# Kernel tuning notes

Hardware: AMD Instinct MI355X
Metric: run time of the kernel (lower is better)

Reference implementation:

```python
import jax, jax.numpy as jnp
import numpy as np

MGC_SIZE = 80
COND_DIM = 256
LSTM_SIZE = 500
UP_SCALE = 64  # prod([4,4,4])
TEMPERATURE = 1.0
EPS_MIN = -7.0


def setup_inputs() -> dict:
    key = jax.random.key(0)
    ks = jax.random.split(key, 10)
    B, T_FRAMES = 16, 32
    T = T_FRAMES * UP_SCALE  # 2048 decode steps
    s = 0.02  # weight scale for numerical stability (logvar goes through exp)
    return {
        "mgc": jax.random.normal(ks[0], (B, T_FRAMES, MGC_SIZE), dtype=jnp.float32),
        "eps": jax.random.normal(ks[1], (B, T), dtype=jnp.float32),
        # UpsampleNet stand-in: linear projection mgc_size->256, then repeat x64 in time
        "W_up": jax.random.normal(ks[2], (MGC_SIZE, COND_DIM), dtype=jnp.float32) * s,
        "b_up": jnp.zeros((COND_DIM,), dtype=jnp.float32),
        # LSTM (PyTorch layout, gate order i,f,g,o)
        "W_ih": jax.random.normal(ks[3], (4 * LSTM_SIZE, COND_DIM + 1), dtype=jnp.float32) * s,
        "W_hh": jax.random.normal(ks[4], (4 * LSTM_SIZE, LSTM_SIZE), dtype=jnp.float32) * s,
        "b_ih": jax.random.normal(ks[5], (4 * LSTM_SIZE,), dtype=jnp.float32) * s,
        "b_hh": jax.random.normal(ks[6], (4 * LSTM_SIZE,), dtype=jnp.float32) * s,
        # output Linear(lstm_size, 2)
        "W_out": jax.random.normal(ks[7], (2, LSTM_SIZE), dtype=jnp.float32) * s,
        "b_out": jnp.zeros((2,), dtype=jnp.float32),
    }


def reference(mgc, eps, W_up, b_up, W_ih, W_hh, b_ih, b_hh, W_out, b_out):
    B = mgc.shape[0]
    # conditioning: (B, T_frames, 80) -> (B, T, 256)
    cond = jnp.repeat(mgc @ W_up + b_up, UP_SCALE, axis=1)
    bias = b_ih + b_hh

    def step(carry, xs):
        h, c, x_prev = carry              # (B,H), (B,H), (B,)
        cond_t, eps_t = xs                # (B,256), (B,)
        inp = jnp.concatenate([cond_t, x_prev[:, None]], axis=1)  # (B,257)
        gates = inp @ W_ih.T + h @ W_hh.T + bias                  # (B,4H)
        i, f, g, o = jnp.split(gates, 4, axis=1)
        i = jax.nn.sigmoid(i)
        f = jax.nn.sigmoid(f)
        g = jnp.tanh(g)
        o = jax.nn.sigmoid(o)
        c = f * c + i * g
        h = o * jnp.tanh(c)
        out = h @ W_out.T + b_out         # (B,2)
        mean = jnp.tanh(out[:, 0])
        logvar = jnp.maximum(out[:, 1], EPS_MIN)  # clamp(min=eps_min)
        zz = mean + (eps_t * TEMPERATURE) * jnp.exp(logvar)
        return (h, c, zz), (mean, logvar, zz)

    h0 = jnp.zeros((B, LSTM_SIZE), dtype=mgc.dtype)
    c0 = jnp.zeros((B, LSTM_SIZE), dtype=mgc.dtype)
    x0 = jnp.zeros((B,), dtype=mgc.dtype)
    xs = (cond.transpose(1, 0, 2), eps.T)  # time-major
    _, (mean, logvar, zz) = jax.lax.scan(step, (h0, c0, x0), xs)
    # back to (B, T)
    return mean.T, logvar.T, zz.T
```

## Files before the change

### kernel.cpp

```cpp
#include <hip/hip_runtime.h>
#include <stdint.h>

#define TSTEPS 2048
#define NB     16
#define HDIM   500
#define HPAD   512
#define NSLICE 16
#define NTHR   256
#define RECU32 320

typedef __attribute__((ext_vector_type(8))) short s16x8;
typedef __attribute__((ext_vector_type(4))) float f32x4;

__device__ __forceinline__ unsigned short f2bf(float f) {
    unsigned u = __float_as_uint(f);
    u += 0x7FFFu + ((u >> 16) & 1u);
    return (unsigned short)(u >> 16);
}
__device__ __forceinline__ float sigm(float x)   { return __fdividef(1.f, 1.f + __expf(-x)); }
__device__ __forceinline__ float tanhf_(float x) { return 1.f - __fdividef(2.f, __expf(2.f * x) + 1.f); }

__global__ void zero_ws_kernel(uint32_t* p, int n) {
    int i = blockIdx.x * blockDim.x + threadIdx.x;
    if (i < n) p[i] = 0u;
}

__global__ __launch_bounds__(NTHR, 1) void wavernn_persist(
    const float* __restrict__ mgc,  const float* __restrict__ eps,
    const float* __restrict__ Wup,  const float* __restrict__ bup,
    const float* __restrict__ Wih,  const float* __restrict__ Whh,
    const float* __restrict__ bih,  const float* __restrict__ bhh,
    const float* __restrict__ Wout, const float* __restrict__ bout,
    float* __restrict__ out, uint32_t* __restrict__ hbuf, uint32_t* __restrict__ seq)
{
    const int s    = blockIdx.x;
    const int tid  = threadIdx.x;
    const int lane = tid & 63;
    const int wave = tid >> 6;
    const int l16  = lane & 15;
    const int g    = lane >> 4;

    __shared__ __align__(16) uint32_t h_sw[HPAD * NB / 2];
    __shared__ __align__(16) float gates_l[NB * 132];
    __shared__ __align__(16) float gcond[128 * NB];
    __shared__ __align__(16) float condT[256 * NB];
    __shared__ __align__(16) float mgcl[NB * 80];
    __shared__ __align__(16) float eps_l[64 * NB];

    s16x8 bfr[2][16];
    float wihl[2];
    #pragma unroll
    for (int t2 = 0; t2 < 2; ++t2) {
        const int q    = t2 * 16 + l16;
        const int hidx = s * 32 + q;
        const bool valid = hidx < HDIM;
        const int grow = wave * HDIM + hidx;
        wihl[t2] = valid ? Wih[grow * 257 + 256] : 0.f;
        #pragma unroll
        for (int kk = 0; kk < 16; ++kk) {
            const int k0 = kk * 32 + g * 8;
            s16x8 r;
            #pragma unroll
            for (int j = 0; j < 8; ++j) {
                const int k = k0 + j;
                const float v = (valid && k < HDIM) ? Whh[grow * HDIM + k] : 0.f;
                r[j] = (short)f2bf(v);
            }
            bfr[t2][kk] = r;
        }
    }
    const int b_e = tid >> 4;
    const int qh  = tid & 15;
    const int q0  = 2 * qh, q1 = q0 + 1;
    const int k0g = s * 32 + q0, k1g = s * 32 + q1;
    const float w0q0 = (k0g < HDIM) ? Wout[k0g]        : 0.f;
    const float w0q1 = (k1g < HDIM) ? Wout[k1g]        : 0.f;
    const float w1q0 = (k0g < HDIM) ? Wout[HDIM + k0g] : 0.f;
    const float w1q1 = (k1g < HDIM) ? Wout[HDIM + k1g] : 0.f;
    const float bout0 = bout[0], bout1 = bout[1];
    float cst0 = 0.f, cst1 = 0.f;

    for (int t = 0; t < TSTEPS; ++t) {
        if (t > 0) {
            int guard = 0;
            while (__hip_atomic_load(&seq[(tid & 15) * 32], __ATOMIC_RELAXED,
                                     __HIP_MEMORY_SCOPE_AGENT) < (uint32_t)t) {
                if (++guard > (1 << 20)) break;
            }
        }
        __threadfence();

        {
            const int b = tid >> 4, p = tid & 15;
            const uint32_t gbase = (uint32_t)((((t & 1) ^ 1) * 16 + p) * RECU32 + b * 16);
            const uint4* srcp = (const uint4*)&hbuf[gbase];
            uint4 v0 = srcp[0], v1 = srcp[1], v2 = srcp[2], v3 = srcp[3];
            const int sw = (b & 7) << 4;
            char* hb = (char*)h_sw;
            *(uint4*)(hb + ((b * 1024 + p * 64 +  0) ^ sw)) = v0;
            *(uint4*)(hb + ((b * 1024 + p * 64 + 16) ^ sw)) = v1;
            *(uint4*)(hb + ((b * 1024 + p * 64 + 32) ^ sw)) = v2;
            *(uint4*)(hb + ((b * 1024 + p * 64 + 48) ^ sw)) = v3;
        }
        float zzv = 0.f, mean = 0.f, lv = 0.f;
        {
            const int b = tid & 15;
            float o0 = bout0, o1 = bout1;
            #pragma unroll
            for (int j = 0; j < 16; ++j) {
                const float2 pp = *(const float2*)&hbuf[(((t & 1) ^ 1) * 16 + j) * RECU32 + 256 + b * 2];
                o0 += pp.x; o1 += pp.y;
            }
            if (t > 0) {
                mean = tanhf_(o0);
                lv   = fmaxf(o1, -7.f);
                zzv  = mean + eps_l[((t - 1) & 63) * NB + b] * __expf(lv);
            }
        }
        if (s == 0 && t > 0 && tid < 16) {
            out[         tid * 2048 + (t - 1)] = mean;
            out[32768 +  tid * 2048 + (t - 1)] = lv;
            out[65536 +  tid * 2048 + (t - 1)] = zzv;
        }
        __syncthreads();

        if ((t & 63) == 0) {
            const int f = t >> 6;
            for (int i = tid; i < NB * 80; i += NTHR) {
                const int b = i / 80, m = i - b * 80;
                mgcl[i] = mgc[(b * 32 + f) * 80 + m];
            }
            for (int i = tid; i < 64 * NB; i += NTHR) {
                const int st = i >> 4, b = i & 15;
                eps_l[i] = eps[b * 2048 + f * 64 + st];
            }
            __syncthreads();
            {
                const int c = tid;
                float a[NB];
                #pragma unroll
                for (int b = 0; b < NB; ++b) a[b] = bup[c];
                for (int m = 0; m < 80; ++m) {
                    const float w = Wup[m * 256 + c];
                    #pragma unroll
                    for (int b = 0; b < NB; ++b) a[b] += mgcl[b * 80 + m] * w;
                }
                #pragma unroll
                for (int b = 0; b < NB; ++b) condT[c * NB + b] = a[b];
            }
            __syncthreads();
            {
                const int n = tid >> 1, kc = tid & 1;
                const int gate = n >> 5, q = n & 31;
                const int hidx = s * 32 + q;
                const bool valid = hidx < HDIM;
                const int grow = gate * HDIM + hidx;
                float a[NB];
                #pragma unroll
                for (int b = 0; b < NB; ++b) a[b] = 0.f;
                if (valid) {
                    const float* wr = Wih + (size_t)grow * 257 + kc * 128;
                    for (int k = 0; k < 128; ++k) {
                        const float w = wr[k];
                        const float* cp = &condT[(kc * 128 + k) * NB];
                        #pragma unroll
                        for (int b = 0; b < NB; ++b) a[b] += cp[b] * w;
                    }
                }
                if (kc == 0) {
                    const float bias = valid ? (bih[grow] + bhh[grow]) : 0.f;
                    #pragma unroll
                    for (int b = 0; b < NB; ++b) gcond[n * NB + b] = a[b] + bias;
                }
                __syncthreads();
                if (kc == 1) {
                    #pragma unroll
                    for (int b = 0; b < NB; ++b) gcond[n * NB + b] += a[b];
                }
            }
            __syncthreads();
        }

        const int n0 = wave * 32 + l16;
        f32x4 acc0a = *(const f32x4*)&gcond[n0 * NB + g * 4];
        f32x4 acc1a = *(const f32x4*)&gcond[(n0 + 16) * NB + g * 4];
        f32x4 acc0b = {0.f, 0.f, 0.f, 0.f};
        f32x4 acc1b = {0.f, 0.f, 0.f, 0.f};
        #pragma unroll
        for (int kk = 0; kk < 8; ++kk) {
            const int off0 = (l16 * 1024 + kk * 64 + g * 16) ^ ((l16 & 7) << 4);
            const int off1 = (l16 * 1024 + (kk + 8) * 64 + g * 16) ^ ((l16 & 7) << 4);
            const s16x8 a0 = *(const s16x8*)((const char*)h_sw + off0);
            const s16x8 a1 = *(const s16x8*)((const char*)h_sw + off1);
            acc0a = __builtin_amdgcn_mfma_f32_16x16x32_bf16(a0, bfr[0][kk],     acc0a, 0, 0, 0);
            acc1a = __builtin_amdgcn_mfma_f32_16x16x32_bf16(a0, bfr[1][kk],     acc1a, 0, 0, 0);
            acc0b = __builtin_amdgcn_mfma_f32_16x16x32_bf16(a1, bfr[0][kk + 8], acc0b, 0, 0, 0);
            acc1b = __builtin_amdgcn_mfma_f32_16x16x32_bf16(a1, bfr[1][kk + 8], acc1b, 0, 0, 0);
        }
        {
            f32x4 zzt;
            zzt[0] = __shfl(zzv, g * 4 + 0);
            zzt[1] = __shfl(zzv, g * 4 + 1);
            zzt[2] = __shfl(zzv, g * 4 + 2);
            zzt[3] = __shfl(zzv, g * 4 + 3);
            const f32x4 r0 = acc0a + acc0b + zzt * wihl[0];
            const f32x4 r1 = acc1a + acc1b + zzt * wihl[1];
            #pragma unroll
            for (int v = 0; v < 4; ++v) {
                gates_l[(g * 4 + v) * 132 + n0]      = r0[v];
                gates_l[(g * 4 + v) * 132 + n0 + 16] = r1[v];
            }
        }
        __syncthreads();

        {
            float po0, po1;
            uint32_t hp = 0;
            {
                const float gi = gates_l[b_e * 132 +      q0];
                const float gf = gates_l[b_e * 132 + 32 + q0];
                const float gg = gates_l[b_e * 132 + 64 + q0];
                const float go = gates_l[b_e * 132 + 96 + q0];
                cst0 = sigm(gf) * cst0 + sigm(gi) * tanhf_(gg);
                const float h = sigm(go) * tanhf_(cst0);
                if (k0g < HDIM) hp |= (uint32_t)f2bf(h);
                po0 = h * w0q0; po1 = h * w1q0;
            }
            {
                const float gi = gates_l[b_e * 132 +      q1];
                const float gf = gates_l[b_e * 132 + 32 + q1];
                const float gg = gates_l[b_e * 132 + 64 + q1];
                const float go = gates_l[b_e * 132 + 96 + q1];
                cst1 = sigm(gf) * cst1 + sigm(gi) * tanhf_(gg);
                const float h = sigm(go) * tanhf_(cst1);
                if (k1g < HDIM) hp |= ((uint32_t)f2bf(h)) << 16;
                po0 += h * w0q1; po1 += h * w1q1;
            }
            const uint32_t rbase = (uint32_t)(((t & 1) * 16 + s) * RECU32);
            __hip_atomic_store(&hbuf[rbase + b_e * 16 + qh], hp,
                               __ATOMIC_RELAXED, __HIP_MEMORY_SCOPE_AGENT);
            po0 += __shfl_xor(po0, 1);  po1 += __shfl_xor(po1, 1);
            po0 += __shfl_xor(po0, 2);  po1 += __shfl_xor(po1, 2);
            po0 += __shfl_xor(po0, 4);  po1 += __shfl_xor(po1, 4);
            po0 += __shfl_xor(po0, 8);  po1 += __shfl_xor(po1, 8);
            if (qh == 0) {
                const uint64_t pk = (uint64_t)__float_as_uint(po0) |
                                    ((uint64_t)__float_as_uint(po1) << 32);
                __hip_atomic_store((uint64_t*)&hbuf[rbase + 256 + b_e * 2], pk,
                                   __ATOMIC_RELAXED, __HIP_MEMORY_SCOPE_AGENT);
            }
        }
        __syncthreads();
        if (tid == 0)
            __hip_atomic_store(&seq[s * 32], (uint32_t)(t + 1),
                               __ATOMIC_RELEASE, __HIP_MEMORY_SCOPE_AGENT);
    }

    if (s == 0) {
        if (tid < 16) {
            int guard = 0;
            while (__hip_atomic_load(&seq[tid * 32], __ATOMIC_RELAXED,
                                     __HIP_MEMORY_SCOPE_AGENT) < (uint32_t)TSTEPS) {
                if (++guard > (1 << 20)) break;
            }
        }
        __syncthreads();
        __threadfence();
        if (tid < 16) {
            float o0 = bout0, o1 = bout1;
            #pragma unroll
            for (int j = 0; j < 16; ++j) {
                const float2 pp = *(const float2*)&hbuf[(16 + j) * RECU32 + 256 + tid * 2];
                o0 += pp.x; o1 += pp.y;
            }
            const float mean = tanhf_(o0);
            const float lvv  = fmaxf(o1, -7.f);
            const float zzv  = mean + eps_l[63 * NB + tid] * __expf(lvv);
            out[         tid * 2048 + 2047] = mean;
            out[32768 +  tid * 2048 + 2047] = lvv;
            out[65536 +  tid * 2048 + 2047] = zzv;
        }
    }
}

extern "C" void kernel_launch(void* const* d_in, const int* in_sizes, int n_in,
                              void* d_out, int out_size, void* d_ws, size_t ws_size,
                              hipStream_t stream) {
    const float* mgc  = (const float*)d_in[0];
    const float* eps  = (const float*)d_in[1];
    const float* Wup  = (const float*)d_in[2];
    const float* bup  = (const float*)d_in[3];
    const float* Wih  = (const float*)d_in[4];
    const float* Whh  = (const float*)d_in[5];
    const float* bih  = (const float*)d_in[6];
    const float* bhh  = (const float*)d_in[7];
    const float* Wout = (const float*)d_in[8];
    const float* bout = (const float*)d_in[9];

    uint32_t* hbuf = (uint32_t*)d_ws;
    uint32_t* seq  = hbuf + 32 * RECU32;

    zero_ws_kernel<<<42, 256, 0, stream>>>(hbuf, 32 * RECU32 + 512);
    wavernn_persist<<<NSLICE, NTHR, 0, stream>>>(mgc, eps, Wup, bup, Wih, Whh,
                                                 bih, bhh, Wout, bout,
                                                 (float*)d_out, hbuf, seq);
}
```

Before: 9.345 ms.

## Load recurrent state straight into MFMA registers and cut per-step barriers

Each wave now polls the sequence flags itself and loads the previous hidden state from global memory straight into MFMA operand registers with atomic loads. This removes the LDS staging copy, the threadfence and one block-wide barrier per step. The output-head reduction moves into wave-level shuffles, and zz is passed through a small LDS array. The conditioning rebuild moves to the end of the step, after the sequence flag is published, and eps is double-buffered so that rebuild overlaps with the other blocks. The cost is more global loads per thread, and the ordering now relies on relaxed atomics plus a compiler barrier rather than an explicit fence.

```diff
diff --git a/kernel.cpp b/kernel.cpp
--- a/kernel.cpp
+++ b/kernel.cpp
@@ -4,10 +4,11 @@
 #define TSTEPS 2048
 #define NB     16
 #define HDIM   500
-#define HPAD   512
 #define NSLICE 16
 #define NTHR   256
 #define RECU32 320
+#define REC64  160
+#define GSTR   20
 
 typedef __attribute__((ext_vector_type(8))) short s16x8;
 typedef __attribute__((ext_vector_type(4))) float f32x4;
@@ -40,12 +41,14 @@
     const int l16  = lane & 15;
     const int g    = lane >> 4;
 
-    __shared__ __align__(16) uint32_t h_sw[HPAD * NB / 2];
     __shared__ __align__(16) float gates_l[NB * 132];
-    __shared__ __align__(16) float gcond[128 * NB];
+    __shared__ __align__(16) float gcond[128 * GSTR];
     __shared__ __align__(16) float condT[256 * NB];
     __shared__ __align__(16) float mgcl[NB * 80];
-    __shared__ __align__(16) float eps_l[64 * NB];
+    __shared__ __align__(16) float eps_l[128 * NB];
+    __shared__ __align__(16) float zz_l[NB];
+
+    uint64_t* hb64all = (uint64_t*)hbuf;
 
     s16x8 bfr[2][16];
     float wihl[2];
@@ -80,136 +83,158 @@
     const float bout0 = bout[0], bout1 = bout[1];
     float cst0 = 0.f, cst1 = 0.f;
 
+    auto rebuild = [&](int f) {
+        for (int i = tid; i < NB * 80; i += NTHR) {
+            const int b = i / 80, m = i - b * 80;
+            mgcl[i] = mgc[(b * 32 + f) * 80 + m];
+        }
+        for (int i = tid; i < 64 * NB; i += NTHR) {
+            const int st = i >> 4, b = i & 15;
+            eps_l[((f & 1) * 64 + st) * NB + b] = eps[b * 2048 + f * 64 + st];
+        }
+        __syncthreads();
+        {
+            const int c = tid;
+            float a[NB];
+            #pragma unroll
+            for (int b = 0; b < NB; ++b) a[b] = bup[c];
+            for (int m = 0; m < 80; ++m) {
+                const float w = Wup[m * 256 + c];
+                #pragma unroll
+                for (int b = 0; b < NB; ++b) a[b] += mgcl[b * 80 + m] * w;
+            }
+            #pragma unroll
+            for (int b = 0; b < NB; ++b) condT[c * NB + b] = a[b];
+        }
+        __syncthreads();
+        {
+            const int n = tid >> 1, kc = tid & 1;
+            const int gate = n >> 5, q = n & 31;
+            const int hidx = s * 32 + q;
+            const bool valid = hidx < HDIM;
+            const int grow = gate * HDIM + hidx;
+            float a[NB];
+            #pragma unroll
+            for (int b = 0; b < NB; ++b) a[b] = 0.f;
+            if (valid) {
+                const float* wr = Wih + (size_t)grow * 257 + kc * 128;
+                for (int k = 0; k < 128; ++k) {
+                    const float w = wr[k];
+                    const float* cp = &condT[(kc * 128 + k) * NB];
+                    #pragma unroll
+                    for (int b = 0; b < NB; ++b) a[b] += cp[b] * w;
+                }
+            }
+            if (kc == 0) {
+                const float bias = valid ? (bih[grow] + bhh[grow]) : 0.f;
+                #pragma unroll
+                for (int b = 0; b < NB; ++b) gcond[n * GSTR + b] = a[b] + bias;
+            }
+            __syncthreads();
+            if (kc == 1) {
+                #pragma unroll
+                for (int b = 0; b < NB; ++b) gcond[n * GSTR + b] += a[b];
+            }
+        }
+        __syncthreads();
+    };
+
+    rebuild(0);
+
     for (int t = 0; t < TSTEPS; ++t) {
         if (t > 0) {
-            int guard = 0;
-            while (__hip_atomic_load(&seq[(tid & 15) * 32], __ATOMIC_RELAXED,
-                                     __HIP_MEMORY_SCOPE_AGENT) < (uint32_t)t) {
-                if (++guard > (1 << 20)) break;
-            }
-        }
-        __threadfence();
-
-        {
-            const int b = tid >> 4, p = tid & 15;
-            const uint32_t gbase = (uint32_t)((((t & 1) ^ 1) * 16 + p) * RECU32 + b * 16);
-            const uint4* srcp = (const uint4*)&hbuf[gbase];
-            uint4 v0 = srcp[0], v1 = srcp[1], v2 = srcp[2], v3 = srcp[3];
-            const int sw = (b & 7) << 4;
-            char* hb = (char*)h_sw;
-            *(uint4*)(hb + ((b * 1024 + p * 64 +  0) ^ sw)) = v0;
-            *(uint4*)(hb + ((b * 1024 + p * 64 + 16) ^ sw)) = v1;
-            *(uint4*)(hb + ((b * 1024 + p * 64 + 32) ^ sw)) = v2;
-            *(uint4*)(hb + ((b * 1024 + p * 64 + 48) ^ sw)) = v3;
-        }
-        float zzv = 0.f, mean = 0.f, lv = 0.f;
-        {
-            const int b = tid & 15;
-            float o0 = bout0, o1 = bout1;
-            #pragma unroll
-            for (int j = 0; j < 16; ++j) {
-                const float2 pp = *(const float2*)&hbuf[(((t & 1) ^ 1) * 16 + j) * RECU32 + 256 + b * 2];
-                o0 += pp.x; o1 += pp.y;
-            }
-            if (t > 0) {
-                mean = tanhf_(o0);
-                lv   = fmaxf(o1, -7.f);
-                zzv  = mean + eps_l[((t - 1) & 63) * NB + b] * __expf(lv);
-            }
-        }
-        if (s == 0 && t > 0 && tid < 16) {
-            out[         tid * 2048 + (t - 1)] = mean;
-            out[32768 +  tid * 2048 + (t - 1)] = lv;
-            out[65536 +  tid * 2048 + (t - 1)] = zzv;
-        }
-        __syncthreads();
-
-        if ((t & 63) == 0) {
-            const int f = t >> 6;
-            for (int i = tid; i < NB * 80; i += NTHR) {
-                const int b = i / 80, m = i - b * 80;
-                mgcl[i] = mgc[(b * 32 + f) * 80 + m];
-            }
-            for (int i = tid; i < 64 * NB; i += NTHR) {
-                const int st = i >> 4, b = i & 15;
-                eps_l[i] = eps[b * 2048 + f * 64 + st];
-            }
-            __syncthreads();
-            {
-                const int c = tid;
-                float a[NB];
-                #pragma unroll
-                for (int b = 0; b < NB; ++b) a[b] = bup[c];
-                for (int m = 0; m < 80; ++m) {
-                    const float w = Wup[m * 256 + c];
-                    #pragma unroll
-                    for (int b = 0; b < NB; ++b) a[b] += mgcl[b * 80 + m] * w;
+            if (lane < 16) {
+                int guard = 0;
+                while (__hip_atomic_load(&seq[lane * 32], __ATOMIC_RELAXED,
+                                         __HIP_MEMORY_SCOPE_AGENT) < (uint32_t)t) {
+                    if (++guard > (1 << 20)) break;
                 }
-                #pragma unroll
-                for (int b = 0; b < NB; ++b) condT[c * NB + b] = a[b];
-            }
-            __syncthreads();
-            {
-                const int n = tid >> 1, kc = tid & 1;
-                const int gate = n >> 5, q = n & 31;
-                const int hidx = s * 32 + q;
-                const bool valid = hidx < HDIM;
-                const int grow = gate * HDIM + hidx;
-                float a[NB];
-                #pragma unroll
-                for (int b = 0; b < NB; ++b) a[b] = 0.f;
-                if (valid) {
-                    const float* wr = Wih + (size_t)grow * 257 + kc * 128;
-                    for (int k = 0; k < 128; ++k) {
-                        const float w = wr[k];
-                        const float* cp = &condT[(kc * 128 + k) * NB];
-                        #pragma unroll
-                        for (int b = 0; b < NB; ++b) a[b] += cp[b] * w;
-                    }
-                }
-                if (kc == 0) {
-                    const float bias = valid ? (bih[grow] + bhh[grow]) : 0.f;
-                    #pragma unroll
-                    for (int b = 0; b < NB; ++b) gcond[n * NB + b] = a[b] + bias;
-                }
-                __syncthreads();
-                if (kc == 1) {
-                    #pragma unroll
-                    for (int b = 0; b < NB; ++b) gcond[n * NB + b] += a[b];
-                }
-            }
-            __syncthreads();
+            }
+            asm volatile("" ::: "memory");
+        }
+
+        uint64_t* hb64 = hb64all + (size_t)(((t & 1) ^ 1) * 16) * REC64;
+        s16x8 hfr[16];
+        #pragma unroll
+        for (int kk = 0; kk < 16; ++kk) {
+            union { uint64_t u[2]; s16x8 v; } hu;
+            hu.u[0] = __hip_atomic_load(hb64 + kk * REC64 + l16 * 8 + g * 2,
+                                        __ATOMIC_RELAXED, __HIP_MEMORY_SCOPE_AGENT);
+            hu.u[1] = __hip_atomic_load(hb64 + kk * REC64 + l16 * 8 + g * 2 + 1,
+                                        __ATOMIC_RELAXED, __HIP_MEMORY_SCOPE_AGENT);
+            hfr[kk] = hu.v;
+        }
+        uint64_t pv[4];
+        if (t > 0) {
+            #pragma unroll
+            for (int j = 0; j < 4; ++j)
+                pv[j] = __hip_atomic_load(hb64 + l16 * REC64 + 128 + g + 4 * j,
+                                          __ATOMIC_RELAXED, __HIP_MEMORY_SCOPE_AGENT);
         }
 
         const int n0 = wave * 32 + l16;
-        f32x4 acc0a = *(const f32x4*)&gcond[n0 * NB + g * 4];
-        f32x4 acc1a = *(const f32x4*)&gcond[(n0 + 16) * NB + g * 4];
+        f32x4 acc0a = *(const f32x4*)&gcond[n0 * GSTR + g * 4];
+        f32x4 acc1a = *(const f32x4*)&gcond[(n0 + 16) * GSTR + g * 4];
         f32x4 acc0b = {0.f, 0.f, 0.f, 0.f};
         f32x4 acc1b = {0.f, 0.f, 0.f, 0.f};
         #pragma unroll
         for (int kk = 0; kk < 8; ++kk) {
-            const int off0 = (l16 * 1024 + kk * 64 + g * 16) ^ ((l16 & 7) << 4);
-            const int off1 = (l16 * 1024 + (kk + 8) * 64 + g * 16) ^ ((l16 & 7) << 4);
-            const s16x8 a0 = *(const s16x8*)((const char*)h_sw + off0);
-            const s16x8 a1 = *(const s16x8*)((const char*)h_sw + off1);
-            acc0a = __builtin_amdgcn_mfma_f32_16x16x32_bf16(a0, bfr[0][kk],     acc0a, 0, 0, 0);
-            acc1a = __builtin_amdgcn_mfma_f32_16x16x32_bf16(a0, bfr[1][kk],     acc1a, 0, 0, 0);
-            acc0b = __builtin_amdgcn_mfma_f32_16x16x32_bf16(a1, bfr[0][kk + 8], acc0b, 0, 0, 0);
-            acc1b = __builtin_amdgcn_mfma_f32_16x16x32_bf16(a1, bfr[1][kk + 8], acc1b, 0, 0, 0);
-        }
-        {
-            f32x4 zzt;
-            zzt[0] = __shfl(zzv, g * 4 + 0);
-            zzt[1] = __shfl(zzv, g * 4 + 1);
-            zzt[2] = __shfl(zzv, g * 4 + 2);
-            zzt[3] = __shfl(zzv, g * 4 + 3);
-            const f32x4 r0 = acc0a + acc0b + zzt * wihl[0];
-            const f32x4 r1 = acc1a + acc1b + zzt * wihl[1];
-            #pragma unroll
-            for (int v = 0; v < 4; ++v) {
-                gates_l[(g * 4 + v) * 132 + n0]      = r0[v];
-                gates_l[(g * 4 + v) * 132 + n0 + 16] = r1[v];
-            }
+            acc0a = __builtin_amdgcn_mfma_f32_16x16x32_bf16(hfr[kk],     bfr[0][kk],     acc0a, 0, 0, 0);
+            acc1a = __builtin_amdgcn_mfma_f32_16x16x32_bf16(hfr[kk],     bfr[1][kk],     acc1a, 0, 0, 0);
+            acc0b = __builtin_amdgcn_mfma_f32_16x16x32_bf16(hfr[kk + 8], bfr[0][kk + 8], acc0b, 0, 0, 0);
+            acc1b = __builtin_amdgcn_mfma_f32_16x16x32_bf16(hfr[kk + 8], bfr[1][kk + 8], acc1b, 0, 0, 0);
+        }
+
+        if (t > 0) {
+            float o0[4], o1[4];
+            #pragma unroll
+            for (int j = 0; j < 4; ++j) {
+                o0[j] = __uint_as_float((uint32_t)pv[j]);
+                o1[j] = __uint_as_float((uint32_t)(pv[j] >> 32));
+            }
+            #pragma unroll
+            for (int m = 1; m < 16; m <<= 1) {
+                #pragma unroll
+                for (int j = 0; j < 4; ++j) {
+                    o0[j] += __shfl_xor(o0[j], m);
+                    o1[j] += __shfl_xor(o1[j], m);
+                }
+            }
+            const int row = (t - 1) & 127;
+            float meanj[4], lvj[4], zzj[4];
+            #pragma unroll
+            for (int j = 0; j < 4; ++j) {
+                const int B = g + 4 * j;
+                meanj[j] = tanhf_(o0[j] + bout0);
+                lvj[j]   = fmaxf(o1[j] + bout1, -7.f);
+                zzj[j]   = meanj[j] + eps_l[row * NB + B] * __expf(lvj[j]);
+            }
+            if (l16 == 0) {
+                #pragma unroll
+                for (int j = 0; j < 4; ++j) zz_l[g + 4 * j] = zzj[j];
+            }
+            if (s == 0 && wave == 0 && l16 == 0) {
+                #pragma unroll
+                for (int j = 0; j < 4; ++j) {
+                    const int B = g + 4 * j;
+                    out[         B * 2048 + (t - 1)] = meanj[j];
+                    out[32768 +  B * 2048 + (t - 1)] = lvj[j];
+                    out[65536 +  B * 2048 + (t - 1)] = zzj[j];
+                }
+            }
+        }
+
+        f32x4 r0 = acc0a + acc0b;
+        f32x4 r1 = acc1a + acc1b;
+        if (t > 0) {
+            const f32x4 zzq = *(const f32x4*)&zz_l[g * 4];
+            r0 += zzq * wihl[0];
+            r1 += zzq * wihl[1];
+        }
+        #pragma unroll
+        for (int v = 0; v < 4; ++v) {
+            gates_l[(g * 4 + v) * 132 + n0]      = r0[v];
+            gates_l[(g * 4 + v) * 132 + n0 + 16] = r1[v];
         }
         __syncthreads();
 
@@ -254,31 +279,47 @@
         if (tid == 0)
             __hip_atomic_store(&seq[s * 32], (uint32_t)(t + 1),
                                __ATOMIC_RELEASE, __HIP_MEMORY_SCOPE_AGENT);
+
+        if (((t + 1) & 63) == 0 && (t + 1) < TSTEPS) rebuild((t + 1) >> 6);
     }
 
-    if (s == 0) {
-        if (tid < 16) {
+    if (s == 0 && wave == 0) {
+        if (lane < 16) {
             int guard = 0;
-            while (__hip_atomic_load(&seq[tid * 32], __ATOMIC_RELAXED,
+            while (__hip_atomic_load(&seq[lane * 32], __ATOMIC_RELAXED,
                                      __HIP_MEMORY_SCOPE_AGENT) < (uint32_t)TSTEPS) {
                 if (++guard > (1 << 20)) break;
             }
         }
-        __syncthreads();
-        __threadfence();
-        if (tid < 16) {
-            float o0 = bout0, o1 = bout1;
-            #pragma unroll
-            for (int j = 0; j < 16; ++j) {
-                const float2 pp = *(const float2*)&hbuf[(16 + j) * RECU32 + 256 + tid * 2];
-                o0 += pp.x; o1 += pp.y;
-            }
-            const float mean = tanhf_(o0);
-            const float lvv  = fmaxf(o1, -7.f);
-            const float zzv  = mean + eps_l[63 * NB + tid] * __expf(lvv);
-            out[         tid * 2048 + 2047] = mean;
-            out[32768 +  tid * 2048 + 2047] = lvv;
-            out[65536 +  tid * 2048 + 2047] = zzv;
+        asm volatile("" ::: "memory");
+        uint64_t* hb64 = hb64all + (size_t)16 * REC64;
+        float o0[4], o1[4];
+        #pragma unroll
+        for (int j = 0; j < 4; ++j) {
+            const uint64_t pvv = __hip_atomic_load(hb64 + l16 * REC64 + 128 + g + 4 * j,
+                                                   __ATOMIC_RELAXED, __HIP_MEMORY_SCOPE_AGENT);
+            o0[j] = __uint_as_float((uint32_t)pvv);
+            o1[j] = __uint_as_float((uint32_t)(pvv >> 32));
+        }
+        #pragma unroll
+        for (int m = 1; m < 16; m <<= 1) {
+            #pragma unroll
+            for (int j = 0; j < 4; ++j) {
+                o0[j] += __shfl_xor(o0[j], m);
+                o1[j] += __shfl_xor(o1[j], m);
+            }
+        }
+        if (l16 == 0) {
+            #pragma unroll
+            for (int j = 0; j < 4; ++j) {
+                const int B = g + 4 * j;
+                const float mean = tanhf_(o0[j] + bout0);
+                const float lvv  = fmaxf(o1[j] + bout1, -7.f);
+                const float zzv  = mean + eps_l[127 * NB + B] * __expf(lvv);
+                out[         B * 2048 + 2047] = mean;
+                out[32768 +  B * 2048 + 2047] = lvv;
+                out[65536 +  B * 2048 + 2047] = zzv;
+            }
         }
     }
 }
```

After: 10.87 ms. 1.16x slower.
